# Kernel optimization log

Measured on AMD Instinct MI355X. Metric: run time of the kernel, lower is better.

The kernel has to match this reference:

```python
import jax, jax.numpy as jnp
import numpy as np

B, N, K, DIM = 1, 50000, 16, 64


def setup_inputs() -> dict:
    key = jax.random.key(0)
    ks = jax.random.split(key, 16)
    s = 0.05  # weight init scale
    return {
        "points_xyz": jax.random.normal(ks[0], (B, N, 3), jnp.float32),
        "points_features": jax.random.normal(ks[1], (B, N, DIM), jnp.float32),
        "neighbours_xyz": jax.random.normal(ks[2], (B, N, K, 3), jnp.float32),
        "neighbours_features": jax.random.normal(ks[3], (B, N, K, DIM), jnp.float32),
        "W_phi": jax.random.normal(ks[4], (DIM, DIM), jnp.float32) * s,
        "b_phi": jnp.zeros((DIM,), jnp.float32),
        "W_psi": jax.random.normal(ks[5], (DIM, DIM), jnp.float32) * s,
        "b_psi": jnp.zeros((DIM,), jnp.float32),
        "W_alpha": jax.random.normal(ks[6], (DIM, DIM), jnp.float32) * s,
        "b_alpha": jnp.zeros((DIM,), jnp.float32),
        "W_gamma": jax.random.normal(ks[7], (DIM, DIM), jnp.float32) * s,
        "b_gamma": jnp.zeros((DIM,), jnp.float32),
        "W_d1": jax.random.normal(ks[8], (3, DIM), jnp.float32) * s,
        "b_d1": jnp.zeros((DIM,), jnp.float32),
        "W_d2": jax.random.normal(ks[9], (DIM, DIM), jnp.float32) * s,
        "b_d2": jnp.zeros((DIM,), jnp.float32),
    }


def reference(points_xyz, points_features, neighbours_xyz, neighbours_features,
              W_phi, b_phi, W_psi, b_psi, W_alpha, b_alpha, W_gamma, b_gamma,
              W_d1, b_d1, W_d2, b_d2):
    # Positional encoding: delta(p_i - p_j) -> (B, N, K, DIM)
    diff = points_xyz[:, :, None, :] - neighbours_xyz          # (B,N,K,3)
    delta = jax.nn.relu((diff @ W_d1 + b_d1) @ W_d2 + b_d2)    # (B,N,K,DIM)

    phi = (points_features @ W_phi + b_phi)[:, :, None, :]     # (B,N,1,DIM)
    psi = neighbours_features @ W_psi + b_psi                  # (B,N,K,DIM)
    beta = phi - psi + delta                                   # (B,N,K,DIM)

    gamma_out = beta @ W_gamma + b_gamma                       # (B,N,K,DIM)
    # NOTE: faithful to source: softmax over the FEATURE axis (dim=-1)
    rho = jax.nn.softmax(gamma_out, axis=-1)                   # (B,N,K,DIM)

    alpha_out = neighbours_features @ W_alpha + b_alpha + delta  # (B,N,K,DIM)
    out = jnp.sum(rho * alpha_out, axis=2)                     # (B,N,DIM)
    return out
```

## Files before the change

### kernel.cpp

```cpp
#include <hip/hip_runtime.h>

typedef unsigned int uint_t;
typedef __attribute__((ext_vector_type(8))) short bf16x8;
typedef __attribute__((ext_vector_type(4))) float f32x4;

#define NPTS 50000
#define DIM  64
#define KNB  16
#define GPW  16
#define NGROUPS (NPTS / GPW)
#define WPB  4
#define NBLOCKS ((NGROUPS + WPB - 1) / WPB)

#define WS_WPA   0
#define WS_WG    4096
#define WS_WPHI  6144
#define WS_WC    8192
#define WS_BC    8384
#define WS_BPP   8448
#define WS_BA    8512
#define WS_BG    8576

__device__ __forceinline__ uint_t rne_pack(float a, float b) {
    uint_t ua = __float_as_uint(a); ua += 0x7fffu + ((ua >> 16) & 1u);
    uint_t ub = __float_as_uint(b); ub += 0x7fffu + ((ub >> 16) & 1u);
    return (ua >> 16) | (ub & 0xffff0000u);
}

union Frag { uint_t u[4]; bf16x8 s; uint4 v; };

__global__ void pt_prep(const float* __restrict__ Wphi, const float* __restrict__ bphi,
                        const float* __restrict__ Wpsi, const float* __restrict__ bpsi,
                        const float* __restrict__ Wa,   const float* __restrict__ ba,
                        const float* __restrict__ Wg,   const float* __restrict__ bg,
                        const float* __restrict__ Wd1,  const float* __restrict__ bd1,
                        const float* __restrict__ Wd2,  const float* __restrict__ bd2,
                        float* __restrict__ ws) {
    int t = threadIdx.x;
    uint_t* wsu = (uint_t*)ws;
    for (int idx = t; idx < 16*64*4; idx += 256) {
        int w = idx & 3, lane = (idx >> 2) & 63, f = idx >> 8;
        int nt = f >> 1, s = f & 1;
        int k = s*32 + (lane >> 4)*8 + 2*w;
        int col = (nt & 3)*16 + (lane & 15);
        const float* W = (nt < 4) ? Wpsi : Wa;
        wsu[WS_WPA + idx] = rne_pack(W[k*64 + col], W[(k+1)*64 + col]);
    }
    for (int idx = t; idx < 8*64*4; idx += 256) {
        int w = idx & 3, lane = (idx >> 2) & 63, f = idx >> 8;
        int nt = f >> 1, s = f & 1;
        int k = s*32 + (lane >> 4)*8 + 2*w;
        int col = nt*16 + (lane & 15);
        wsu[WS_WG   + idx] = rne_pack(Wg[k*64 + col],   Wg[(k+1)*64 + col]);
        wsu[WS_WPHI + idx] = rne_pack(Wphi[k*64 + col], Wphi[(k+1)*64 + col]);
    }
    if (t < DIM) {
        for (int c = 0; c < 3; ++c) {
            float acc = 0.f;
            for (int m = 0; m < DIM; ++m) acc += Wd1[c*DIM + m] * Wd2[m*DIM + t];
            ws[WS_WC + c*DIM + t] = acc;
        }
        float acc = bd2[t];
        for (int m = 0; m < DIM; ++m) acc += bd1[m] * Wd2[m*DIM + t];
        ws[WS_BC  + t] = acc;
        ws[WS_BPP + t] = bphi[t] - bpsi[t];
        ws[WS_BA  + t] = ba[t];
        ws[WS_BG  + t] = bg[t];
    }
}

#define MFMA(A, B, C) __builtin_amdgcn_mfma_f32_16x16x32_bf16((A), (B), (C), 0, 0, 0)

#define PHI_SZ (16*65)
#define BTR_SZ (64*17)
#define WAREA  (PHI_SZ + BTR_SZ + 64)

__global__ __launch_bounds__(256, 2)
void pt_main(const float* __restrict__ pxyz, const float* __restrict__ pfeat,
             const float* __restrict__ nxyz, const float* __restrict__ nfeat,
             const float* __restrict__ ws,   float* __restrict__ out) {
    __shared__ uint4 wlds[16*64];
    __shared__ float warea[WPB][WAREA];

    const int t    = threadIdx.x;
    const int wv   = t >> 6;
    const int lane = t & 63;
    const int c16  = lane & 15;
    const int quad = lane >> 4;

    {
        const uint4* src = (const uint4*)((const uint_t*)ws + WS_WG);
        for (int i = t; i < 16*64; i += 256) wlds[i] = src[i];
    }
    __syncthreads();

    const int g = blockIdx.x * WPB + wv;
    if (g >= NGROUPS) return;

    float* phi_s = &warea[wv][0];
    float* btr   = phi_s + PHI_SZ;
    float* dxyz  = btr + BTR_SZ;

    Frag bpa[16];
    #pragma unroll
    for (int f = 0; f < 16; ++f)
        bpa[f].v = ((const uint4*)((const uint_t*)ws + WS_WPA))[f*64 + lane];

    float wcx[4], wcy[4], wcz[4], wbc[4], bar[4], bgr[4], bppr[4];
    #pragma unroll
    for (int nt = 0; nt < 4; ++nt) {
        int d = nt*16 + c16;
        wcx[nt]  = ws[WS_WC + d];
        wcy[nt]  = ws[WS_WC + 64 + d];
        wcz[nt]  = ws[WS_WC + 128 + d];
        wbc[nt]  = ws[WS_BC + d];
        bppr[nt] = ws[WS_BPP + d];
        bar[nt]  = ws[WS_BA + d];
        bgr[nt]  = ws[WS_BG + d];
    }

    const int g0 = g * GPW;

    {
        const float* base = pfeat + (size_t)(g0 + c16)*DIM + quad*8;
        float4 x0 = *(const float4*)(base);
        float4 x1 = *(const float4*)(base + 4);
        float4 x2 = *(const float4*)(base + 32);
        float4 x3 = *(const float4*)(base + 36);
        Frag a0, a1;
        a0.u[0] = rne_pack(x0.x, x0.y); a0.u[1] = rne_pack(x0.z, x0.w);
        a0.u[2] = rne_pack(x1.x, x1.y); a0.u[3] = rne_pack(x1.z, x1.w);
        a1.u[0] = rne_pack(x2.x, x2.y); a1.u[1] = rne_pack(x2.z, x2.w);
        a1.u[2] = rne_pack(x3.x, x3.y); a1.u[3] = rne_pack(x3.z, x3.w);
        #pragma unroll
        for (int nt = 0; nt < 4; ++nt) {
            f32x4 acc = {bppr[nt], bppr[nt], bppr[nt], bppr[nt]};
            Frag b0, b1;
            b0.v = wlds[512 + (nt*2 + 0)*64 + lane];
            b1.v = wlds[512 + (nt*2 + 1)*64 + lane];
            acc = MFMA(a0.s, b0.s, acc);
            acc = MFMA(a1.s, b1.s, acc);
            #pragma unroll
            for (int r = 0; r < 4; ++r)
                phi_s[(quad*4 + r)*65 + nt*16 + c16] = acc[r];
        }
    }

    float4 x0, x1, x2, x3; float nv = 0.f;
    {
        const float* nfb = nfeat + ((size_t)g0*KNB + c16)*DIM + quad*8;
        x0 = *(const float4*)(nfb);
        x1 = *(const float4*)(nfb + 4);
        x2 = *(const float4*)(nfb + 32);
        x3 = *(const float4*)(nfb + 36);
        if (lane < 48) nv = nxyz[(size_t)g0*KNB*3 + lane];
    }

    #pragma unroll 1
    for (int i = 0; i < GPW; ++i) {
        const int n = g0 + i;
        const size_t pbase = (size_t)n * KNB;

        float4 c0 = x0, c1 = x1, c2 = x2, c3 = x3;
        float cnv = nv;

        if (i + 1 < GPW) {
            const float* nfb = nfeat + (pbase + KNB + c16)*DIM + quad*8;
            x0 = *(const float4*)(nfb);
            x1 = *(const float4*)(nfb + 4);
            x2 = *(const float4*)(nfb + 32);
            x3 = *(const float4*)(nfb + 36);
            if (lane < 48) nv = nxyz[(pbase + KNB)*3 + lane];
        }

        {
            float p0 = pxyz[n*3], p1 = pxyz[n*3+1], p2 = pxyz[n*3+2];
            if (lane < 48) {
                int pr = lane / 3, comp = lane - pr*3;
                float px = (comp == 0) ? p0 : ((comp == 1) ? p1 : p2);
                dxyz[lane] = px - cnv;
            }
        }

        Frag na0, na1;
        na0.u[0] = rne_pack(c0.x, c0.y); na0.u[1] = rne_pack(c0.z, c0.w);
        na0.u[2] = rne_pack(c1.x, c1.y); na0.u[3] = rne_pack(c1.z, c1.w);
        na1.u[0] = rne_pack(c2.x, c2.y); na1.u[1] = rne_pack(c2.z, c2.w);
        na1.u[2] = rne_pack(c3.x, c3.y); na1.u[3] = rne_pack(c3.z, c3.w);

        f32x4 acc[8];
        #pragma unroll
        for (int nt = 0; nt < 8; ++nt) {
            float iv = (nt < 4) ? 0.f : bar[nt-4];
            acc[nt] = f32x4{iv, iv, iv, iv};
        }
        #pragma unroll
        for (int nt = 0; nt < 8; ++nt) {
            acc[nt] = MFMA(na0.s, bpa[nt*2 + 0].s, acc[nt]);
            acc[nt] = MFMA(na1.s, bpa[nt*2 + 1].s, acc[nt]);
        }

        float dx[4], dy[4], dz[4];
        #pragma unroll
        for (int r = 0; r < 4; ++r) {
            int m = quad*4 + r;
            dx[r] = dxyz[m*3]; dy[r] = dxyz[m*3+1]; dz[r] = dxyz[m*3+2];
        }
        float alpha[4][4];
        #pragma unroll
        for (int nt = 0; nt < 4; ++nt) {
            float phv = phi_s[i*65 + nt*16 + c16];
            #pragma unroll
            for (int r = 0; r < 4; ++r) {
                float del = fmaxf(dx[r]*wcx[nt] + dy[r]*wcy[nt] + dz[r]*wcz[nt] + wbc[nt], 0.f);
                float beta = phv - acc[nt][r] + del;
                alpha[nt][r] = acc[nt+4][r] + del;
                btr[(nt*16 + c16)*17 + quad*4 + r] = beta;
            }
        }

        Frag ga0, ga1;
        #pragma unroll
        for (int w = 0; w < 4; ++w) {
            int j = 2*w;
            float f0 = btr[(quad*8 + j    )*17 + c16];
            float f1 = btr[(quad*8 + j + 1)*17 + c16];
            float f2 = btr[(32 + quad*8 + j    )*17 + c16];
            float f3 = btr[(32 + quad*8 + j + 1)*17 + c16];
            ga0.u[w] = rne_pack(f0, f1);
            ga1.u[w] = rne_pack(f2, f3);
        }
        f32x4 gacc[4];
        #pragma unroll
        for (int nt = 0; nt < 4; ++nt) gacc[nt] = f32x4{bgr[nt], bgr[nt], bgr[nt], bgr[nt]};
        #pragma unroll
        for (int nt = 0; nt < 4; ++nt) {
            Frag b0, b1;
            b0.v = wlds[(nt*2 + 0)*64 + lane];
            b1.v = wlds[(nt*2 + 1)*64 + lane];
            gacc[nt] = MFMA(ga0.s, b0.s, gacc[nt]);
            gacc[nt] = MFMA(ga1.s, b1.s, gacc[nt]);
        }

        float rho[4][4], smi[4];
        #pragma unroll
        for (int r = 0; r < 4; ++r) {
            float mx = fmaxf(fmaxf(gacc[0][r], gacc[1][r]), fmaxf(gacc[2][r], gacc[3][r]));
            #pragma unroll
            for (int d = 1; d < 16; d <<= 1) mx = fmaxf(mx, __shfl_xor(mx, d));
            float s = 0.f;
            #pragma unroll
            for (int nt = 0; nt < 4; ++nt) { float e = __expf(gacc[nt][r] - mx); rho[nt][r] = e; s += e; }
            #pragma unroll
            for (int d = 1; d < 16; d <<= 1) s += __shfl_xor(s, d);
            smi[r] = __builtin_amdgcn_rcpf(s);
        }

        float outp[4];
        #pragma unroll
        for (int nt = 0; nt < 4; ++nt) {
            float p = 0.f;
            #pragma unroll
            for (int r = 0; r < 4; ++r) p += rho[nt][r] * smi[r] * alpha[nt][r];
            p += __shfl_xor(p, 16);
            p += __shfl_xor(p, 32);
            outp[nt] = p;
        }
        float sel = (quad == 0) ? outp[0] : (quad == 1) ? outp[1] : (quad == 2) ? outp[2] : outp[3];
        out[(size_t)n*DIM + lane] = sel;
    }
}

extern "C" void kernel_launch(void* const* d_in, const int* in_sizes, int n_in,
                              void* d_out, int out_size, void* d_ws, size_t ws_size,
                              hipStream_t stream) {
    const float* pxyz  = (const float*)d_in[0];
    const float* pfeat = (const float*)d_in[1];
    const float* nxyz  = (const float*)d_in[2];
    const float* nfeat = (const float*)d_in[3];
    const float* Wphi  = (const float*)d_in[4];
    const float* bphi  = (const float*)d_in[5];
    const float* Wpsi  = (const float*)d_in[6];
    const float* bpsi  = (const float*)d_in[7];
    const float* Wa    = (const float*)d_in[8];
    const float* ba    = (const float*)d_in[9];
    const float* Wg    = (const float*)d_in[10];
    const float* bg    = (const float*)d_in[11];
    const float* Wd1   = (const float*)d_in[12];
    const float* bd1   = (const float*)d_in[13];
    const float* Wd2   = (const float*)d_in[14];
    const float* bd2   = (const float*)d_in[15];
    float* ws = (float*)d_ws;

    pt_prep<<<1, 256, 0, stream>>>(Wphi, bphi, Wpsi, bpsi, Wa, ba, Wg, bg,
                                   Wd1, bd1, Wd2, bd2, ws);
    pt_main<<<NBLOCKS, 256, 0, stream>>>(pxyz, pfeat, nxyz, nfeat, ws, (float*)d_out);
}
```

Baseline: 381.1 us.

## Fold W_gamma into phi/psi weights and drop softmax max subtraction

Precomputes Wphi·Wg and -Wpsi·Wg (plus combined bias) in a parallel prep kernel. gamma_out then comes directly from MFMAs on the neighbour features and the positional term, so beta is no longer materialised and the psi projection is gone. The delta term is passed to the gamma MFMA through a permuted bf16 LDS tile. The group size is halved, the weight tile moves from LDS to registers, and the softmax max reduction is removed, which risks overflow in exp for large logits. Folding the weights also shifts bf16 rounding points, which changes numerics.

```diff
diff --git a/kernel.cpp b/kernel.cpp
--- a/kernel.cpp
+++ b/kernel.cpp
@@ -1,4 +1,5 @@
 #include <hip/hip_runtime.h>
+#include <hip/hip_bf16.h>
 
 typedef unsigned int uint_t;
 typedef __attribute__((ext_vector_type(8))) short bf16x8;
@@ -7,27 +8,31 @@
 #define NPTS 50000
 #define DIM  64
 #define KNB  16
-#define GPW  16
+#define GPW  8
 #define NGROUPS (NPTS / GPW)
 #define WPB  4
 #define NBLOCKS ((NGROUPS + WPB - 1) / WPB)
 
-#define WS_WPA   0
-#define WS_WG    4096
-#define WS_WPHI  6144
-#define WS_WC    8192
-#define WS_BC    8384
-#define WS_BPP   8448
-#define WS_BA    8512
-#define WS_BG    8576
-
-__device__ __forceinline__ uint_t rne_pack(float a, float b) {
-    uint_t ua = __float_as_uint(a); ua += 0x7fffu + ((ua >> 16) & 1u);
-    uint_t ub = __float_as_uint(b); ub += 0x7fffu + ((ub >> 16) & 1u);
-    return (ua >> 16) | (ub & 0xffff0000u);
+#define FR_WA    0
+#define FR_PSIG  2048
+#define FR_WG    4096
+#define FR_PHIG  6144
+#define WC4      8192
+#define GB       8448
+#define BA       8512
+
+__device__ __forceinline__ uint_t pk(float a, float b) {
+    union { __hip_bfloat162 h; uint_t u; } cv;
+    cv.h = __float22bfloat162_rn(float2{a, b});
+    return cv.u;
 }
 
 union Frag { uint_t u[4]; bf16x8 s; uint4 v; };
+
+__device__ __forceinline__ int sigma(int k) {
+    int t = k >> 1;
+    return (t & 15) + 32 * (t >> 4) + 16 * (k & 1);
+}
 
 __global__ void pt_prep(const float* __restrict__ Wphi, const float* __restrict__ bphi,
                         const float* __restrict__ Wpsi, const float* __restrict__ bpsi,
@@ -36,51 +41,72 @@
                         const float* __restrict__ Wd1,  const float* __restrict__ bd1,
                         const float* __restrict__ Wd2,  const float* __restrict__ bd2,
                         float* __restrict__ ws) {
-    int t = threadIdx.x;
+    int b = blockIdx.x, t = threadIdx.x;
     uint_t* wsu = (uint_t*)ws;
-    for (int idx = t; idx < 16*64*4; idx += 256) {
-        int w = idx & 3, lane = (idx >> 2) & 63, f = idx >> 8;
-        int nt = f >> 1, s = f & 1;
-        int k = s*32 + (lane >> 4)*8 + 2*w;
-        int col = (nt & 3)*16 + (lane & 15);
-        const float* W = (nt < 4) ? Wpsi : Wa;
-        wsu[WS_WPA + idx] = rne_pack(W[k*64 + col], W[(k+1)*64 + col]);
-    }
-    for (int idx = t; idx < 8*64*4; idx += 256) {
-        int w = idx & 3, lane = (idx >> 2) & 63, f = idx >> 8;
-        int nt = f >> 1, s = f & 1;
-        int k = s*32 + (lane >> 4)*8 + 2*w;
-        int col = nt*16 + (lane & 15);
-        wsu[WS_WG   + idx] = rne_pack(Wg[k*64 + col],   Wg[(k+1)*64 + col]);
-        wsu[WS_WPHI + idx] = rne_pack(Wphi[k*64 + col], Wphi[(k+1)*64 + col]);
-    }
-    if (t < DIM) {
-        for (int c = 0; c < 3; ++c) {
-            float acc = 0.f;
-            for (int m = 0; m < DIM; ++m) acc += Wd1[c*DIM + m] * Wd2[m*DIM + t];
-            ws[WS_WC + c*DIM + t] = acc;
-        }
-        float acc = bd2[t];
-        for (int m = 0; m < DIM; ++m) acc += bd1[m] * Wd2[m*DIM + t];
-        ws[WS_BC  + t] = acc;
-        ws[WS_BPP + t] = bphi[t] - bpsi[t];
-        ws[WS_BA  + t] = ba[t];
-        ws[WS_BG  + t] = bg[t];
+    if (b < 32) {
+        int gid  = b * 256 + t;
+        int img  = gid >> 11;
+        int rem  = gid & 2047;
+        int f    = rem >> 8;
+        int lane = (rem >> 2) & 63;
+        int w    = rem & 3;
+        int k0   = (f & 1) * 32 + (lane >> 4) * 8 + 2 * w;
+        int k1   = k0 + 1;
+        int n    = (f >> 1) * 16 + (lane & 15);
+        float v0, v1;
+        if (img == 0) {
+            v0 = Wa[k0 * 64 + n]; v1 = Wa[k1 * 64 + n];
+            wsu[FR_WA + rem] = pk(v0, v1);
+        } else if (img == 1) {
+            float a0 = 0.f, a1 = 0.f;
+            for (int c = 0; c < 64; ++c) {
+                float wgc = Wg[c * 64 + n];
+                a0 += Wpsi[k0 * 64 + c] * wgc;
+                a1 += Wpsi[k1 * 64 + c] * wgc;
+            }
+            wsu[FR_PSIG + rem] = pk(-a0, -a1);
+        } else if (img == 2) {
+            v0 = Wg[sigma(k0) * 64 + n]; v1 = Wg[sigma(k1) * 64 + n];
+            wsu[FR_WG + rem] = pk(v0, v1);
+        } else {
+            float a0 = 0.f, a1 = 0.f;
+            for (int c = 0; c < 64; ++c) {
+                float wgc = Wg[c * 64 + n];
+                a0 += Wphi[k0 * 64 + c] * wgc;
+                a1 += Wphi[k1 * 64 + c] * wgc;
+            }
+            wsu[FR_PHIG + rem] = pk(a0, a1);
+        }
+    } else if (t < 64) {
+        float wx = 0.f, wy = 0.f, wz = 0.f;
+        for (int m = 0; m < 64; ++m) {
+            float w2 = Wd2[m * 64 + t];
+            wx += Wd1[m] * w2;
+            wy += Wd1[64 + m] * w2;
+            wz += Wd1[128 + m] * w2;
+        }
+        float wb = bd2[t];
+        for (int m = 0; m < 64; ++m) wb += bd1[m] * Wd2[m * 64 + t];
+        ws[WC4 + t * 4 + 0] = wx;
+        ws[WC4 + t * 4 + 1] = wy;
+        ws[WC4 + t * 4 + 2] = wz;
+        ws[WC4 + t * 4 + 3] = wb;
+        float g = bg[t];
+        for (int c = 0; c < 64; ++c) g += (bphi[c] - bpsi[c]) * Wg[c * 64 + t];
+        ws[GB + t] = g;
+        ws[BA + t] = ba[t];
     }
 }
 
 #define MFMA(A, B, C) __builtin_amdgcn_mfma_f32_16x16x32_bf16((A), (B), (C), 0, 0, 0)
 
-#define PHI_SZ (16*65)
-#define BTR_SZ (64*17)
-#define WAREA  (PHI_SZ + BTR_SZ + 64)
+#define WAREA 1224
 
 __global__ __launch_bounds__(256, 2)
 void pt_main(const float* __restrict__ pxyz, const float* __restrict__ pfeat,
              const float* __restrict__ nxyz, const float* __restrict__ nfeat,
              const float* __restrict__ ws,   float* __restrict__ out) {
-    __shared__ uint4 wlds[16*64];
-    __shared__ float warea[WPB][WAREA];
+    __shared__ float lds[WPB][WAREA];
 
     const int t    = threadIdx.x;
     const int wv   = t >> 6;
@@ -88,186 +114,184 @@
     const int c16  = lane & 15;
     const int quad = lane >> 4;
 
-    {
-        const uint4* src = (const uint4*)((const uint_t*)ws + WS_WG);
-        for (int i = t; i < 16*64; i += 256) wlds[i] = src[i];
-    }
-    __syncthreads();
-
     const int g = blockIdx.x * WPB + wv;
     if (g >= NGROUPS) return;
 
-    float* phi_s = &warea[wv][0];
-    float* btr   = phi_s + PHI_SZ;
-    float* dxyz  = btr + BTR_SZ;
-
-    Frag bpa[16];
+    float*  phig_s = &lds[wv][0];
+    uint_t* utr    = (uint_t*)(phig_s + 520);
+    float*  dxyz   = (float*)(utr + 544);
+    float*  pxyz_s = dxyz + 128;
+
+    const uint4* fr = (const uint4*)ws;
+    Frag wa[8], wpsig[8], wg[8];
     #pragma unroll
-    for (int f = 0; f < 16; ++f)
-        bpa[f].v = ((const uint4*)((const uint_t*)ws + WS_WPA))[f*64 + lane];
-
-    float wcx[4], wcy[4], wcz[4], wbc[4], bar[4], bgr[4], bppr[4];
+    for (int f = 0; f < 8; ++f) {
+        wa[f].v    = fr[           f * 64 + lane];
+        wpsig[f].v = fr[ 512 +     f * 64 + lane];
+        wg[f].v    = fr[1024 +     f * 64 + lane];
+    }
+    float4 wc[4];
+    float ba_r[4], gbr[4];
     #pragma unroll
     for (int nt = 0; nt < 4; ++nt) {
-        int d = nt*16 + c16;
-        wcx[nt]  = ws[WS_WC + d];
-        wcy[nt]  = ws[WS_WC + 64 + d];
-        wcz[nt]  = ws[WS_WC + 128 + d];
-        wbc[nt]  = ws[WS_BC + d];
-        bppr[nt] = ws[WS_BPP + d];
-        bar[nt]  = ws[WS_BA + d];
-        bgr[nt]  = ws[WS_BG + d];
+        int d = nt * 16 + c16;
+        wc[nt]   = ((const float4*)(ws + WC4))[d];
+        ba_r[nt] = ws[BA + d];
+        gbr[nt]  = ws[GB + d];
     }
 
     const int g0 = g * GPW;
+    const int k3 = lane / 3, c3 = lane - k3 * 3;
+
+    if (lane < 24) pxyz_s[lane] = pxyz[g0 * 3 + lane];
+    float nv0 = (lane < 48) ? nxyz[(size_t)g0 * 48 + lane] : 0.f;
+    if (lane < 48) dxyz[k3 * 4 + c3] = pxyz_s[c3] - nv0;
 
     {
-        const float* base = pfeat + (size_t)(g0 + c16)*DIM + quad*8;
-        float4 x0 = *(const float4*)(base);
-        float4 x1 = *(const float4*)(base + 4);
-        float4 x2 = *(const float4*)(base + 32);
-        float4 x3 = *(const float4*)(base + 36);
-        Frag a0, a1;
-        a0.u[0] = rne_pack(x0.x, x0.y); a0.u[1] = rne_pack(x0.z, x0.w);
-        a0.u[2] = rne_pack(x1.x, x1.y); a0.u[3] = rne_pack(x1.z, x1.w);
-        a1.u[0] = rne_pack(x2.x, x2.y); a1.u[1] = rne_pack(x2.z, x2.w);
-        a1.u[2] = rne_pack(x3.x, x3.y); a1.u[3] = rne_pack(x3.z, x3.w);
-        #pragma unroll
-        for (int nt = 0; nt < 4; ++nt) {
-            f32x4 acc = {bppr[nt], bppr[nt], bppr[nt], bppr[nt]};
+        float4 x0{}, x1{}, x2{}, x3{};
+        if (c16 < 8) {
+            const float* base = pfeat + (size_t)(g0 + c16) * 64 + quad * 8;
+            x0 = *(const float4*)(base);
+            x1 = *(const float4*)(base + 4);
+            x2 = *(const float4*)(base + 32);
+            x3 = *(const float4*)(base + 36);
+        }
+        Frag pa0, pa1;
+        pa0.u[0] = pk(x0.x, x0.y); pa0.u[1] = pk(x0.z, x0.w);
+        pa0.u[2] = pk(x1.x, x1.y); pa0.u[3] = pk(x1.z, x1.w);
+        pa1.u[0] = pk(x2.x, x2.y); pa1.u[1] = pk(x2.z, x2.w);
+        pa1.u[2] = pk(x3.x, x3.y); pa1.u[3] = pk(x3.z, x3.w);
+        #pragma unroll
+        for (int nt = 0; nt < 4; ++nt) {
             Frag b0, b1;
-            b0.v = wlds[512 + (nt*2 + 0)*64 + lane];
-            b1.v = wlds[512 + (nt*2 + 1)*64 + lane];
-            acc = MFMA(a0.s, b0.s, acc);
-            acc = MFMA(a1.s, b1.s, acc);
-            #pragma unroll
-            for (int r = 0; r < 4; ++r)
-                phi_s[(quad*4 + r)*65 + nt*16 + c16] = acc[r];
-        }
-    }
-
-    float4 x0, x1, x2, x3; float nv = 0.f;
-    {
-        const float* nfb = nfeat + ((size_t)g0*KNB + c16)*DIM + quad*8;
-        x0 = *(const float4*)(nfb);
-        x1 = *(const float4*)(nfb + 4);
-        x2 = *(const float4*)(nfb + 32);
-        x3 = *(const float4*)(nfb + 36);
-        if (lane < 48) nv = nxyz[(size_t)g0*KNB*3 + lane];
-    }
+            b0.v = fr[1536 + (nt * 2 + 0) * 64 + lane];
+            b1.v = fr[1536 + (nt * 2 + 1) * 64 + lane];
+            f32x4 acc = {gbr[nt], gbr[nt], gbr[nt], gbr[nt]};
+            acc = MFMA(pa0.s, b0.s, acc);
+            acc = MFMA(pa1.s, b1.s, acc);
+            if (quad < 2) {
+                #pragma unroll
+                for (int r = 0; r < 4; ++r)
+                    phig_s[(quad * 4 + r) * 65 + nt * 16 + c16] = acc[r];
+            }
+        }
+    }
+
+    const float* nfb = nfeat + (size_t)g0 * (KNB * 64) + (size_t)c16 * 64 + quad * 8;
+    float4 f0 = *(const float4*)(nfb);
+    float4 f1 = *(const float4*)(nfb + 4);
+    float4 f2 = *(const float4*)(nfb + 32);
+    float4 f3 = *(const float4*)(nfb + 36);
+    float nvn = (lane < 48) ? nxyz[(size_t)g0 * 48 + 48 + lane] : 0.f;
 
     #pragma unroll 1
     for (int i = 0; i < GPW; ++i) {
         const int n = g0 + i;
-        const size_t pbase = (size_t)n * KNB;
-
-        float4 c0 = x0, c1 = x1, c2 = x2, c3 = x3;
-        float cnv = nv;
-
+
+        Frag na0, na1;
+        na0.u[0] = pk(f0.x, f0.y); na0.u[1] = pk(f0.z, f0.w);
+        na0.u[2] = pk(f1.x, f1.y); na0.u[3] = pk(f1.z, f1.w);
+        na1.u[0] = pk(f2.x, f2.y); na1.u[1] = pk(f2.z, f2.w);
+        na1.u[2] = pk(f3.x, f3.y); na1.u[3] = pk(f3.z, f3.w);
         if (i + 1 < GPW) {
-            const float* nfb = nfeat + (pbase + KNB + c16)*DIM + quad*8;
-            x0 = *(const float4*)(nfb);
-            x1 = *(const float4*)(nfb + 4);
-            x2 = *(const float4*)(nfb + 32);
-            x3 = *(const float4*)(nfb + 36);
-            if (lane < 48) nv = nxyz[(pbase + KNB)*3 + lane];
-        }
-
-        {
-            float p0 = pxyz[n*3], p1 = pxyz[n*3+1], p2 = pxyz[n*3+2];
-            if (lane < 48) {
-                int pr = lane / 3, comp = lane - pr*3;
-                float px = (comp == 0) ? p0 : ((comp == 1) ? p1 : p2);
-                dxyz[lane] = px - cnv;
-            }
-        }
-
-        Frag na0, na1;
-        na0.u[0] = rne_pack(c0.x, c0.y); na0.u[1] = rne_pack(c0.z, c0.w);
-        na0.u[2] = rne_pack(c1.x, c1.y); na0.u[3] = rne_pack(c1.z, c1.w);
-        na1.u[0] = rne_pack(c2.x, c2.y); na1.u[1] = rne_pack(c2.z, c2.w);
-        na1.u[2] = rne_pack(c3.x, c3.y); na1.u[3] = rne_pack(c3.z, c3.w);
-
-        f32x4 acc[8];
-        #pragma unroll
-        for (int nt = 0; nt < 8; ++nt) {
-            float iv = (nt < 4) ? 0.f : bar[nt-4];
-            acc[nt] = f32x4{iv, iv, iv, iv};
-        }
-        #pragma unroll
-        for (int nt = 0; nt < 8; ++nt) {
-            acc[nt] = MFMA(na0.s, bpa[nt*2 + 0].s, acc[nt]);
-            acc[nt] = MFMA(na1.s, bpa[nt*2 + 1].s, acc[nt]);
-        }
-
-        float dx[4], dy[4], dz[4];
-        #pragma unroll
-        for (int r = 0; r < 4; ++r) {
-            int m = quad*4 + r;
-            dx[r] = dxyz[m*3]; dy[r] = dxyz[m*3+1]; dz[r] = dxyz[m*3+2];
-        }
-        float alpha[4][4];
-        #pragma unroll
-        for (int nt = 0; nt < 4; ++nt) {
-            float phv = phi_s[i*65 + nt*16 + c16];
+            const float* nf2 = nfb + (size_t)(i + 1) * (KNB * 64);
+            f0 = *(const float4*)(nf2);
+            f1 = *(const float4*)(nf2 + 4);
+            f2 = *(const float4*)(nf2 + 32);
+            f3 = *(const float4*)(nf2 + 36);
+        }
+
+        float ph[4];
+        #pragma unroll
+        for (int nt = 0; nt < 4; ++nt) ph[nt] = phig_s[i * 65 + nt * 16 + c16];
+        float4 dd[4];
+        #pragma unroll
+        for (int r = 0; r < 4; ++r)
+            dd[r] = ((const float4*)dxyz)[(i & 1) * 16 + quad * 4 + r];
+
+        if (i + 1 < GPW) {
+            if (lane < 48)
+                dxyz[((i + 1) & 1) * 64 + k3 * 4 + c3] = pxyz_s[(i + 1) * 3 + c3] - nvn;
+            if (i + 2 < GPW)
+                nvn = (lane < 48) ? nxyz[((size_t)n + 2) * 48 + lane] : 0.f;
+        }
+
+        float d_c[4][4];
+        #pragma unroll
+        for (int nt = 0; nt < 4; ++nt) {
             #pragma unroll
             for (int r = 0; r < 4; ++r) {
-                float del = fmaxf(dx[r]*wcx[nt] + dy[r]*wcy[nt] + dz[r]*wcz[nt] + wbc[nt], 0.f);
-                float beta = phv - acc[nt][r] + del;
-                alpha[nt][r] = acc[nt+4][r] + del;
-                btr[(nt*16 + c16)*17 + quad*4 + r] = beta;
+                float u = fmaf(dd[r].x, wc[nt].x,
+                          fmaf(dd[r].y, wc[nt].y,
+                          fmaf(dd[r].z, wc[nt].z, wc[nt].w)));
+                d_c[nt][r] = fmaxf(u, 0.f);
             }
         }
-
-        Frag ga0, ga1;
-        #pragma unroll
-        for (int w = 0; w < 4; ++w) {
-            int j = 2*w;
-            float f0 = btr[(quad*8 + j    )*17 + c16];
-            float f1 = btr[(quad*8 + j + 1)*17 + c16];
-            float f2 = btr[(32 + quad*8 + j    )*17 + c16];
-            float f3 = btr[(32 + quad*8 + j + 1)*17 + c16];
-            ga0.u[w] = rne_pack(f0, f1);
-            ga1.u[w] = rne_pack(f2, f3);
+        #pragma unroll
+        for (int r = 0; r < 4; ++r) {
+            int row = (quad * 4 + r) * 34;
+            utr[row + c16]      = pk(d_c[0][r], d_c[1][r]);
+            utr[row + 16 + c16] = pk(d_c[2][r], d_c[3][r]);
+        }
+
+        f32x4 aacc[4];
+        #pragma unroll
+        for (int nt = 0; nt < 4; ++nt) {
+            aacc[nt] = f32x4{ba_r[nt], ba_r[nt], ba_r[nt], ba_r[nt]};
+            aacc[nt] = MFMA(na0.s, wa[nt * 2 + 0].s, aacc[nt]);
+            aacc[nt] = MFMA(na1.s, wa[nt * 2 + 1].s, aacc[nt]);
         }
         f32x4 gacc[4];
         #pragma unroll
-        for (int nt = 0; nt < 4; ++nt) gacc[nt] = f32x4{bgr[nt], bgr[nt], bgr[nt], bgr[nt]};
-        #pragma unroll
-        for (int nt = 0; nt < 4; ++nt) {
-            Frag b0, b1;
-            b0.v = wlds[(nt*2 + 0)*64 + lane];
-            b1.v = wlds[(nt*2 + 1)*64 + lane];
-            gacc[nt] = MFMA(ga0.s, b0.s, gacc[nt]);
-            gacc[nt] = MFMA(ga1.s, b1.s, gacc[nt]);
-        }
-
-        float rho[4][4], smi[4];
+        for (int nt = 0; nt < 4; ++nt) {
+            gacc[nt] = f32x4{ph[nt], ph[nt], ph[nt], ph[nt]};
+            gacc[nt] = MFMA(na0.s, wpsig[nt * 2 + 0].s, gacc[nt]);
+            gacc[nt] = MFMA(na1.s, wpsig[nt * 2 + 1].s, gacc[nt]);
+        }
+        Frag da0, da1;
+        {
+            const uint_t* rowp = utr + c16 * 34 + quad * 4;
+            uint2 a = *(const uint2*)(rowp);
+            uint2 b = *(const uint2*)(rowp + 2);
+            uint2 c = *(const uint2*)(rowp + 16);
+            uint2 d = *(const uint2*)(rowp + 18);
+            da0.u[0] = a.x; da0.u[1] = a.y; da0.u[2] = b.x; da0.u[3] = b.y;
+            da1.u[0] = c.x; da1.u[1] = c.y; da1.u[2] = d.x; da1.u[3] = d.y;
+        }
+        #pragma unroll
+        for (int nt = 0; nt < 4; ++nt) {
+            gacc[nt] = MFMA(da0.s, wg[nt * 2 + 0].s, gacc[nt]);
+            gacc[nt] = MFMA(da1.s, wg[nt * 2 + 1].s, gacc[nt]);
+        }
+        #pragma unroll
+        for (int nt = 0; nt < 4; ++nt)
+            #pragma unroll
+            for (int r = 0; r < 4; ++r) aacc[nt][r] += d_c[nt][r];
+
+        float e[4][4], smi[4];
         #pragma unroll
         for (int r = 0; r < 4; ++r) {
-            float mx = fmaxf(fmaxf(gacc[0][r], gacc[1][r]), fmaxf(gacc[2][r], gacc[3][r]));
-            #pragma unroll
-            for (int d = 1; d < 16; d <<= 1) mx = fmaxf(mx, __shfl_xor(mx, d));
             float s = 0.f;
             #pragma unroll
-            for (int nt = 0; nt < 4; ++nt) { float e = __expf(gacc[nt][r] - mx); rho[nt][r] = e; s += e; }
+            for (int nt = 0; nt < 4; ++nt) { e[nt][r] = __expf(gacc[nt][r]); s += e[nt][r]; }
             #pragma unroll
-            for (int d = 1; d < 16; d <<= 1) s += __shfl_xor(s, d);
+            for (int d2 = 1; d2 < 16; d2 <<= 1) s += __shfl_xor(s, d2);
             smi[r] = __builtin_amdgcn_rcpf(s);
         }
-
-        float outp[4];
-        #pragma unroll
-        for (int nt = 0; nt < 4; ++nt) {
-            float p = 0.f;
-            #pragma unroll
-            for (int r = 0; r < 4; ++r) p += rho[nt][r] * smi[r] * alpha[nt][r];
-            p += __shfl_xor(p, 16);
-            p += __shfl_xor(p, 32);
-            outp[nt] = p;
-        }
-        float sel = (quad == 0) ? outp[0] : (quad == 1) ? outp[1] : (quad == 2) ? outp[2] : outp[3];
-        out[(size_t)n*DIM + lane] = sel;
+        float p0 = 0.f, p1 = 0.f, p2 = 0.f, p3 = 0.f;
+        #pragma unroll
+        for (int r = 0; r < 4; ++r) {
+            p0 = fmaf(e[0][r] * smi[r], aacc[0][r], p0);
+            p1 = fmaf(e[1][r] * smi[r], aacc[1][r], p1);
+            p2 = fmaf(e[2][r] * smi[r], aacc[2][r], p2);
+            p3 = fmaf(e[3][r] * smi[r], aacc[3][r], p3);
+        }
+        p0 += __shfl_xor(p0, 16); p0 += __shfl_xor(p0, 32);
+        p1 += __shfl_xor(p1, 16); p1 += __shfl_xor(p1, 32);
+        p2 += __shfl_xor(p2, 16); p2 += __shfl_xor(p2, 32);
+        p3 += __shfl_xor(p3, 16); p3 += __shfl_xor(p3, 32);
+        float sel = (quad == 0) ? p0 : (quad == 1) ? p1 : (quad == 2) ? p2 : p3;
+        out[(size_t)n * 64 + lane] = sel;
     }
 }
 
@@ -292,7 +316,7 @@
     const float* bd2   = (const float*)d_in[15];
     float* ws = (float*)d_ws;
 
-    pt_prep<<<1, 256, 0, stream>>>(Wphi, bphi, Wpsi, bpsi, Wa, ba, Wg, bg,
-                                   Wd1, bd1, Wd2, bd2, ws);
+    pt_prep<<<33, 256, 0, stream>>>(Wphi, bphi, Wpsi, bpsi, Wa, ba, Wg, bg,
+                                    Wd1, bd1, Wd2, bd2, ws);
     pt_main<<<NBLOCKS, 256, 0, stream>>>(pxyz, pfeat, nxyz, nfeat, ws, (float*)d_out);
 }
```

After: 347.1 us. -8.9%, faster.
